# Performance work log

Measured on AMD Instinct MI355X. Metric: run time of the kernel, lower is better.

The kernel has to match this reference:

```python
import jax, jax.numpy as jnp
import numpy as np

B, SQ, SV = 2, 2048, 2048
DV, DQ, DK, DO, H = 1024, 1280, 1024, 1024, 16
DHK, DHO = DK // H, DO // H


def setup_inputs() -> dict:
    key = jax.random.key(0)
    ks = jax.random.split(key, 8)
    pre_value_key = jax.random.normal(ks[0], (B, SV, DV), jnp.float32)
    pre_query = jax.random.normal(ks[1], (B, SQ, DQ), jnp.float32)
    value_key_masks = (jax.random.uniform(ks[2], (B, SV)) < 0.9).astype(jnp.float32)
    value_key_counts = jnp.maximum(value_key_masks.sum(-1), 1.0)
    s = 0.02
    Wq = jax.random.normal(ks[3], (DQ, DK), jnp.float32) * s
    bq = jnp.zeros((DK,), jnp.float32)
    Wk = jax.random.normal(ks[4], (DV, DK), jnp.float32) * s
    bk = jnp.zeros((DK,), jnp.float32)
    Wv = jax.random.normal(ks[5], (DV, DO), jnp.float32) * s
    bv = jnp.zeros((DO,), jnp.float32)
    overall_gain = jnp.ones((1, H, 1, 1), jnp.float32)
    overall_bias = jnp.full((1, H, 1, 1), -10.0, jnp.float32)
    return dict(pre_value_key=pre_value_key, pre_query=pre_query,
                value_key_masks=value_key_masks, value_key_counts=value_key_counts,
                Wq=Wq, bq=bq, Wk=Wk, bk=bk, Wv=Wv, bv=bv,
                overall_gain=overall_gain, overall_bias=overall_bias)


def _heads(x, h):
    # (B, S, D) -> (B, h, S, D//h)
    b, s, d = x.shape
    return x.reshape(b, s, h, d // h).transpose(0, 2, 1, 3)


def reference(pre_value_key, pre_query, value_key_masks, value_key_counts,
              Wq, bq, Wk, bk, Wv, bv, overall_gain, overall_bias):
    q = _heads(pre_query @ Wq + bq, H)        # (B,H,SQ,DHK)
    k = _heads(pre_value_key @ Wk + bk, H)    # (B,H,SV,DHK)
    v = _heads(pre_value_key @ Wv + bv, H)    # (B,H,SV,DHO)

    scores = jnp.einsum('bhqd,bhkd->bhqk', q, k) / jnp.sqrt(jnp.float32(DHK))

    mask = value_key_masks  # (B,SV), 0/1 float
    # pooled-score sigmoid gate (cross-attn branch)
    pooled = (scores * mask[:, None, None, :]).sum(-1, keepdims=True)
    pooled = pooled / value_key_counts[:, None, None, None]
    overall_weight = jax.nn.sigmoid(pooled * overall_gain + overall_bias)  # (B,H,SQ,1)

    add_mask = jnp.where(mask == 0, -jnp.inf, 0.0).astype(scores.dtype)
    sm = jax.nn.softmax(scores + add_mask[:, None, None, :], axis=-1)
    h = jnp.einsum('bhqk,bhkd->bhqd', sm, v)  # (B,H,SQ,DHO)

    pq_split = _heads(pre_query[:, :, :DO], H)  # (B,H,SQ,DHO)
    out = pq_split * (1.0 - overall_weight) + h * overall_weight
    out = out.transpose(0, 2, 1, 3).reshape(B, SQ, DO)
    out = jnp.concatenate([out, pre_query[:, :, DO:]], axis=-1)  # (B,SQ,DQ)
    return out
```

## Files before the change

### kernel.cpp

```cpp
#include <hip/hip_runtime.h>

typedef __attribute__((ext_vector_type(8))) __bf16 bf16x8;
typedef __attribute__((ext_vector_type(4))) float f32x4;
typedef __attribute__((ext_vector_type(16))) float f32x16;
typedef __attribute__((ext_vector_type(4))) unsigned short us4;
typedef __attribute__((ext_vector_type(4))) unsigned int u32x4;
typedef __attribute__((ext_vector_type(2))) unsigned int u32x2;
typedef __attribute__((address_space(3))) void* as3vp;
typedef const __attribute__((address_space(1))) void* as1vp;

#define GLOAD_LDS16(g, l) __builtin_amdgcn_global_load_lds((as1vp)(g), (as3vp)(l), 16, 0, 0)

#if __has_builtin(__builtin_amdgcn_exp2f)
#define EXP2(x) __builtin_amdgcn_exp2f(x)
#else
#define EXP2(x) __expf((x) * 0.6931471805599453f)
#endif

__device__ __forceinline__ unsigned short f2bf(float f) {
  unsigned u = __builtin_bit_cast(unsigned, f);
  u += 0x7FFFu + ((u >> 16) & 1u);
  return (unsigned short)(u >> 16);
}
__device__ __forceinline__ float bf2f(unsigned short u) {
  return __builtin_bit_cast(float, (unsigned)u << 16);
}
__device__ __forceinline__ unsigned int pkbf(float a, float b) {
  unsigned int r;
  asm("v_cvt_pk_bf16_f32 %0, %1, %2" : "=v"(r) : "v"(a), "v"(b));
  return r;
}

__global__ void cvt_pq_tail(const float* __restrict__ x, unsigned short* __restrict__ y,
                            float* __restrict__ out) {
  const int i = blockIdx.x * 256 + threadIdx.x;
  if (i >= 1310720) return;
  float4 v = ((const float4*)x)[i];
  us4 o;
  o.x = f2bf(v.x); o.y = f2bf(v.y); o.z = f2bf(v.z); o.w = f2bf(v.w);
  ((us4*)y)[i] = o;
  if ((i % 320) >= 256) ((float4*)out)[i] = v;
}

__global__ void cvt_f32_bf16(const float* __restrict__ x, unsigned short* __restrict__ y, int n4) {
  int i = blockIdx.x * 256 + threadIdx.x;
  if (i >= n4) return;
  float4 v = ((const float4*)x)[i];
  us4 o;
  o.x = f2bf(v.x); o.y = f2bf(v.y); o.z = f2bf(v.z); o.w = f2bf(v.w);
  ((us4*)y)[i] = o;
}

__global__ void transpose_w3(const float* __restrict__ Wq, const float* __restrict__ Wk,
                             const float* __restrict__ Wv,
                             unsigned short* __restrict__ WqT, unsigned short* __restrict__ WkT,
                             unsigned short* __restrict__ WvT) {
  const int z = blockIdx.z;
  const int K = (z == 0) ? 1280 : 1024;
  if ((int)blockIdx.y * 32 >= K) return;
  const float* W = (z == 0) ? Wq : ((z == 1) ? Wk : Wv);
  unsigned short* WT = (z == 0) ? WqT : ((z == 1) ? WkT : WvT);
  __shared__ float t[32][33];
  const int tx = threadIdx.x & 31, ty = threadIdx.x >> 5;
  const int n0 = blockIdx.x * 32, k0 = blockIdx.y * 32;
#pragma unroll
  for (int i = 0; i < 32; i += 8)
    t[ty + i][tx] = W[(size_t)(k0 + ty + i) * 1024 + n0 + tx];
  __syncthreads();
#pragma unroll
  for (int i = 0; i < 32; i += 8)
    WT[(size_t)(n0 + ty + i) * K + k0 + tx] = f2bf(t[tx][ty + i]);
}

__global__ void km_reduce(const unsigned short* __restrict__ KF, const float* __restrict__ mask,
                          float* __restrict__ km, unsigned short* __restrict__ addm_bf) {
  if (blockIdx.x < 16) {
    const int i = blockIdx.x * 256 + threadIdx.x;
    addm_bf[i] = f2bf((mask[i] != 0.f) ? 0.f : -1e30f);
  }
  __shared__ float red[16][64];
  const int bh = blockIdx.x >> 3, chunk = blockIdx.x & 7;
  const int b = bh >> 4;
  const int dg = (threadIdx.x & 15) * 4, rg = threadIdx.x >> 4;
  const unsigned short* kfb = KF + ((size_t)bh << 17);
  const float* mr = mask + b * 2048;
  const int ks = dg >> 4, h5 = (dg >> 3) & 1, j0 = dg & 7;
  float a0 = 0.f, a1 = 0.f, a2 = 0.f, a3 = 0.f;
  const int kv0 = chunk * 256;
  for (int kv = kv0 + rg; kv < kv0 + 256; kv += 16) {
    const float mv = mr[kv];
    const int t = kv >> 6, rowin = kv & 63;
    const size_t off = (size_t)(((t * 4 + ks) * 2 + (rowin >> 5)) * 64 + h5 * 32 + (rowin & 31)) * 8 + j0;
    us4 kq = *(const us4*)(kfb + off);
    a0 = fmaf(mv, bf2f(kq.x), a0); a1 = fmaf(mv, bf2f(kq.y), a1);
    a2 = fmaf(mv, bf2f(kq.z), a2); a3 = fmaf(mv, bf2f(kq.w), a3);
  }
  red[rg][dg] = a0; red[rg][dg + 1] = a1; red[rg][dg + 2] = a2; red[rg][dg + 3] = a3;
  __syncthreads();
  if (threadIdx.x < 64) {
    float s = 0.f;
#pragma unroll
    for (int i = 0; i < 16; ++i) s += red[i][threadIdx.x];
    atomicAdd(&km[bh * 64 + threadIdx.x], s);
  }
}

__global__ __launch_bounds__(256, 2)
void gemm_all(const unsigned short* __restrict__ Aq,
              const unsigned short* __restrict__ Akv,
              const unsigned short* __restrict__ WqT,
              const unsigned short* __restrict__ WkT,
              const unsigned short* __restrict__ WvT,
              const float* __restrict__ bq,
              const float* __restrict__ bk,
              const float* __restrict__ bv,
              unsigned short* __restrict__ Qout,
              unsigned short* __restrict__ KFout,
              unsigned short* __restrict__ VFout) {
  __shared__ unsigned short sA[2][128 * 64];
  __shared__ unsigned short sB[2][128 * 64];
  const int z = blockIdx.z;
  const int KDIM = (z == 0) ? 1280 : 1024;
  const unsigned short* Arow = (z == 0) ? Aq : ((z == 1) ? WkT : Akv);
  const unsigned short* Brow = (z == 0) ? WqT : ((z == 1) ? Akv : WvT);
  const int rowA0 = (z == 1) ? blockIdx.y * 128 : blockIdx.x * 128;
  const int rowB0 = (z == 1) ? blockIdx.x * 128 : blockIdx.y * 128;

  const int tid = threadIdx.x, lane = tid & 63, w = tid >> 6;
  const int l15 = lane & 15, lhi = lane >> 4;
  const int wm = w >> 1, wn = w & 1;

  const f32x4 zv = {0.f, 0.f, 0.f, 0.f};
  f32x4 acc[4][4];
#pragma unroll
  for (int m = 0; m < 4; ++m)
#pragma unroll
    for (int n = 0; n < 4; ++n) acc[m][n] = zv;

  auto stage = [&](int buf, int kt) {
#pragma unroll
    for (int i = 0; i < 4; ++i) {
      const int c = i * 256 + tid;
      const int r = c >> 3, kc = ((c & 7) ^ (r & 7)) * 8;
      GLOAD_LDS16(Arow + (size_t)(rowA0 + r) * KDIM + kt + kc, &sA[buf][0] + c * 8);
      GLOAD_LDS16(Brow + (size_t)(rowB0 + r) * KDIM + kt + kc, &sB[buf][0] + c * 8);
    }
  };

  const int NT = KDIM / 64;
  stage(0, 0);
  __syncthreads();
  int cur = 0;
  for (int t = 0; t < NT; ++t) {
    if (t + 1 < NT) stage(cur ^ 1, (t + 1) * 64);
    const unsigned short* sAb = &sA[cur][0];
    const unsigned short* sBb = &sB[cur][0];
#pragma unroll
    for (int ks = 0; ks < 2; ++ks) {
      const int koS = (ks * 32 + lhi * 8) ^ ((l15 & 7) * 8);
      bf16x8 af[4], bfr[4];
#pragma unroll
      for (int m = 0; m < 4; ++m) af[m] = *(const bf16x8*)(sAb + (wm * 64 + m * 16 + l15) * 64 + koS);
#pragma unroll
      for (int n = 0; n < 4; ++n) bfr[n] = *(const bf16x8*)(sBb + (wn * 64 + n * 16 + l15) * 64 + koS);
#pragma unroll
      for (int m = 0; m < 4; ++m)
#pragma unroll
        for (int n = 0; n < 4; ++n)
          acc[m][n] = __builtin_amdgcn_mfma_f32_16x16x32_bf16(af[m], bfr[n], acc[m][n], 0, 0, 0);
    }
    __syncthreads();
    cur ^= 1;
  }

  if (z == 0) {
#pragma unroll
    for (int n = 0; n < 4; ++n) {
      const int gc = rowB0 + wn * 64 + n * 16 + l15;
      const float bb = bq[gc];
#pragma unroll
      for (int m = 0; m < 4; ++m) {
        const int gr0 = rowA0 + wm * 64 + m * 16 + lhi * 4;
#pragma unroll
        for (int r = 0; r < 4; ++r)
          Qout[(size_t)(gr0 + r) * 1024 + gc] = f2bf((acc[m][n][r] + bb) * 0.18033688f);
      }
    }
  } else if (z == 1) {
#pragma unroll
    for (int n = 0; n < 4; ++n) {
      const int gkv = rowB0 + wn * 64 + n * 16 + l15;
      const int b = gkv >> 11, kvl = gkv & 2047;
      const int t = kvl >> 6, rowin = kvl & 63;
      const int halfk = rowin >> 5, l31k = rowin & 31;
#pragma unroll
      for (int m = 0; m < 4; ++m) {
        const int gch = rowA0 + wm * 64 + m * 16 + lhi * 4;
        const f32x4 bb = *(const f32x4*)(bk + gch);
        const int h = gch >> 6, chh = gch & 63;
        const int ks = chh >> 4, h5k = (chh >> 3) & 1, j0 = chh & 7;
        const size_t off = ((size_t)(b * 16 + h) << 17) +
                           (size_t)(((t * 4 + ks) * 2 + halfk) * 64 + h5k * 32 + l31k) * 8 + j0;
        u32x2 st;
        st.x = pkbf(acc[m][n][0] + bb[0], acc[m][n][1] + bb[1]);
        st.y = pkbf(acc[m][n][2] + bb[2], acc[m][n][3] + bb[3]);
        *(u32x2*)(KFout + off) = st;
      }
    }
  } else {
    __syncthreads();
    unsigned* tb = (unsigned*)&sA[0][0];
#pragma unroll
    for (int n = 0; n < 4; ++n) {
      const int gcL = wn * 64 + n * 16 + l15;
      const float bb = bv[rowB0 + gcL];
#pragma unroll
      for (int m = 0; m < 4; ++m) {
#pragma unroll
        for (int k = 0; k < 2; ++k) {
          const int grPair = wm * 32 + m * 8 + lhi * 2 + k;
          const int W = (grPair & 3) | ((((grPair >> 2) ^ gcL) & 15) << 2);
          tb[gcL * 64 + W] = pkbf(acc[m][n][2 * k] + bb, acc[m][n][2 * k + 1] + bb);
        }
      }
    }
    __syncthreads();
    const int b_ = rowA0 >> 11;
#pragma unroll
    for (int it = 0; it < 8; ++it) {
      const int c = it * 256 + tid;
      const int gcL = (c & 63) + ((c >> 10) << 6);
      const int u = (c >> 6) & 15;
      const int W4 = (u ^ gcL) & 15;
      u32x4 o = *(const u32x4*)(tb + gcL * 64 + W4 * 4);
      const int kv0 = (rowA0 & 2047) + u * 8;
      const int ch = rowB0 + gcL;
      const int hh2 = ch >> 6, d = ch & 63;
      const int t2 = kv0 >> 6, ks2 = (kv0 >> 4) & 3, h5v = (kv0 >> 3) & 1;
      const size_t off = ((size_t)(b_ * 16 + hh2) << 17) +
                         (size_t)(((t2 * 4 + ks2) * 2 + (d >> 5)) * 64 + h5v * 32 + (d & 31)) * 8;
      *(u32x4*)(VFout + off) = o;
    }
  }
}

__global__ __launch_bounds__(256, 2)
void attn_fused(const unsigned short* __restrict__ Q,
                const unsigned short* __restrict__ KF,
                const unsigned short* __restrict__ VF,
                const unsigned short* __restrict__ addm_bf,
                const float* __restrict__ km,
                const float* __restrict__ counts,
                const float* __restrict__ gain,
                const float* __restrict__ gbias,
                const float* __restrict__ pq,
                float* __restrict__ out) {
  __shared__ float sOT[4 * 2048];

  const int tid = threadIdx.x, lane = tid & 63, w = tid >> 6;
  const int l31 = lane & 31, h5 = lane >> 5;
  const int f = blockIdx.x;
  const int qt = (f >> 3) & 15;
  const int bh = (f & 7) + 8 * (f >> 7);
  const int b = bh >> 4, hh = bh & 15;
  const int q0 = qt * 128;

  bf16x8 qf[4];
  {
    const unsigned short* qp = Q + (size_t)(b * 2048 + q0 + w * 32 + l31) * 1024 + hh * 64 + h5 * 8;
#pragma unroll
    for (int ks = 0; ks < 4; ++ks) qf[ks] = *(const bf16x8*)(qp + ks * 16);
  }

  float pl_s = 0.f;
  {
    const float* kmp = km + (b * 16 + hh) * 64 + h5 * 8;
#pragma unroll
    for (int ks = 0; ks < 4; ++ks) {
      f32x4 ka = *(const f32x4*)(kmp + ks * 16);
      f32x4 kb4 = *(const f32x4*)(kmp + ks * 16 + 4);
#pragma unroll
      for (int j = 0; j < 4; ++j)
        pl_s += (float)qf[ks][j] * ka[j] + (float)qf[ks][j + 4] * kb4[j];
    }
    float ta = pl_s, tb = pl_s;
    asm("v_permlane32_swap_b32 %0, %1" : "+v"(ta), "+v"(tb));
    pl_s = ta + tb;
  }

  const unsigned short* KFb = KF + ((size_t)bh << 17) + lane * 8;
  const unsigned short* VFb = VF + ((size_t)bh << 17) + lane * 8;
  const unsigned short* amb = addm_bf + b * 2048;

  bf16x8 qone;
  {
    u32x4 fq = {h5 ? 0u : 0x3F80u, 0u, 0u, 0u};
    qone = __builtin_bit_cast(bf16x8, fq);
  }

  f32x16 o0, o1, l_vec;
#pragma unroll
  for (int r = 0; r < 16; ++r) { o0[r] = 0.f; o1[r] = 0.f; l_vec[r] = 0.f; }
  float m_ = -1e30f;

  bf16x8 kA[8], kB[8], vf[8];
  auto ldK = [&](int t, bf16x8 (&kf)[8]) {
    const unsigned short* p = KFb + (size_t)t * 4096;
#pragma unroll
    for (int i = 0; i < 8; ++i) kf[i] = *(const bf16x8*)(p + i * 512);
  };
  auto ldV = [&](int t, bf16x8 (&vv)[8]) {
    const unsigned short* p = VFb + (size_t)t * 4096;
#pragma unroll
    for (int i = 0; i < 8; ++i) vv[i] = *(const bf16x8*)(p + i * 512);
  };

  auto body = [&](int t, bf16x8 (&kf)[8], bf16x8 (&nkf)[8], bool ln) {
    ldV(t, vf);
    if (ln) ldK(t + 1, nkf);
    const unsigned short am0 = amb[t * 64 + l31];
    const unsigned short am1 = amb[t * 64 + 32 + l31];

    f32x16 s0, s1;
#pragma unroll
    for (int r = 0; r < 16; ++r) { s0[r] = 0.f; s1[r] = 0.f; }

#pragma unroll
    for (int ks = 0; ks < 4; ++ks) {
      s0 = __builtin_amdgcn_mfma_f32_32x32x16_bf16(kf[ks * 2], qf[ks], s0, 0, 0, 0);
      s1 = __builtin_amdgcn_mfma_f32_32x32x16_bf16(kf[ks * 2 + 1], qf[ks], s1, 0, 0, 0);
    }
    {
      u32x4 fa0 = {h5 ? 0u : (unsigned)am0, 0u, 0u, 0u};
      u32x4 fa1 = {h5 ? 0u : (unsigned)am1, 0u, 0u, 0u};
      s0 = __builtin_amdgcn_mfma_f32_32x32x16_bf16(__builtin_bit_cast(bf16x8, fa0), qone, s0, 0, 0, 0);
      s1 = __builtin_amdgcn_mfma_f32_32x32x16_bf16(__builtin_bit_cast(bf16x8, fa1), qone, s1, 0, 0, 0);
    }

    f32x16 mx;
#pragma unroll
    for (int r = 0; r < 16; ++r) mx[r] = fmaxf(s0[r], s1[r]);
    float t8[8];
#pragma unroll
    for (int r = 0; r < 8; ++r) t8[r] = fmaxf(mx[r], mx[r + 8]);
    float tp = fmaxf(fmaxf(fmaxf(t8[0], t8[1]), fmaxf(t8[2], t8[3])),
                     fmaxf(fmaxf(t8[4], t8[5]), fmaxf(t8[6], t8[7])));
    {
      float ta = tp, tb = tp;
      asm("v_permlane32_swap_b32 %0, %1" : "+v"(ta), "+v"(tb));
      tp = fmaxf(ta, tb);
    }
    if (__any(tp > m_ + 11.0f)) {
      const float mnew = fmaxf(m_, tp);
      const float corr = EXP2(m_ - mnew);
      m_ = mnew;
      l_vec *= corr; o0 *= corr; o1 *= corr;
    }

    f32x16 p0, p1;
#pragma unroll
    for (int r = 0; r < 16; ++r) p0[r] = EXP2(s0[r] - m_);
#pragma unroll
    for (int r = 0; r < 16; ++r) p1[r] = EXP2(s1[r] - m_);
    l_vec += p0; l_vec += p1;

    bf16x8 pfs[4];
    {
      unsigned x0 = pkbf(p0[0], p0[1]), y0 = pkbf(p0[2], p0[3]);
      unsigned z0 = pkbf(p0[4], p0[5]), w0 = pkbf(p0[6], p0[7]);
      asm("v_permlane32_swap_b32 %0, %1" : "+v"(x0), "+v"(z0));
      asm("v_permlane32_swap_b32 %0, %1" : "+v"(y0), "+v"(w0));
      u32x4 f0 = {x0, y0, z0, w0};
      pfs[0] = __builtin_bit_cast(bf16x8, f0);
      unsigned x1 = pkbf(p0[8], p0[9]), y1 = pkbf(p0[10], p0[11]);
      unsigned z1 = pkbf(p0[12], p0[13]), w1 = pkbf(p0[14], p0[15]);
      asm("v_permlane32_swap_b32 %0, %1" : "+v"(x1), "+v"(z1));
      asm("v_permlane32_swap_b32 %0, %1" : "+v"(y1), "+v"(w1));
      u32x4 f1 = {x1, y1, z1, w1};
      pfs[1] = __builtin_bit_cast(bf16x8, f1);
      unsigned x2 = pkbf(p1[0], p1[1]), y2 = pkbf(p1[2], p1[3]);
      unsigned z2 = pkbf(p1[4], p1[5]), w2 = pkbf(p1[6], p1[7]);
      asm("v_permlane32_swap_b32 %0, %1" : "+v"(x2), "+v"(z2));
      asm("v_permlane32_swap_b32 %0, %1" : "+v"(y2), "+v"(w2));
      u32x4 f2 = {x2, y2, z2, w2};
      pfs[2] = __builtin_bit_cast(bf16x8, f2);
      unsigned x3 = pkbf(p1[8], p1[9]), y3 = pkbf(p1[10], p1[11]);
      unsigned z3 = pkbf(p1[12], p1[13]), w3 = pkbf(p1[14], p1[15]);
      asm("v_permlane32_swap_b32 %0, %1" : "+v"(x3), "+v"(z3));
      asm("v_permlane32_swap_b32 %0, %1" : "+v"(y3), "+v"(w3));
      u32x4 f3 = {x3, y3, z3, w3};
      pfs[3] = __builtin_bit_cast(bf16x8, f3);
    }

#pragma unroll
    for (int ks = 0; ks < 4; ++ks) {
      o0 = __builtin_amdgcn_mfma_f32_32x32x16_bf16(vf[ks * 2], pfs[ks], o0, 0, 0, 0);
      o1 = __builtin_amdgcn_mfma_f32_32x32x16_bf16(vf[ks * 2 + 1], pfs[ks], o1, 0, 0, 0);
    }
  };

  ldK(0, kA);
#pragma unroll 1
  for (int t = 0; t < 32; t += 2) {
    body(t, kA, kB, true);
    body(t + 1, kB, kA, t + 2 < 32);
  }

  float l_s;
  {
    float a[8];
#pragma unroll
    for (int r = 0; r < 8; ++r) a[r] = l_vec[r] + l_vec[r + 8];
    l_s = ((a[0] + a[1]) + (a[2] + a[3])) + ((a[4] + a[5]) + (a[6] + a[7]));
    float ta = l_s, tb = l_s;
    asm("v_permlane32_swap_b32 %0, %1" : "+v"(ta), "+v"(tb));
    l_s = ta + tb;
  }
  const float po = pl_s * 0.6931471805599453f / counts[b];
  const float wgv = 1.f / (1.f + __expf(-(po * gain[hh] + gbias[hh])));
  const float invl = 1.f / l_s;

  float* myOT = sOT + w * 2048;
#pragma unroll
  for (int r = 0; r < 16; ++r) {
    const int d0 = (r & 3) + 8 * (r >> 2) + 4 * h5;
    myOT[d0 * 32 + (l31 ^ (d0 & 31))] = o0[r] * invl;
    const int d1 = d0 + 32;
    myOT[d1 * 32 + (l31 ^ (d1 & 31))] = o1[r] * invl;
  }
  __syncthreads();
  const size_t rowbase = (size_t)(b * 2048 + q0 + w * 32) * 1280 + hh * 64 + lane;
  const float* pqrow = pq + rowbase;
  float* outrow = out + rowbase;
#pragma unroll 4
  for (int i = 0; i < 32; ++i) {
    const float hval = myOT[lane * 32 + (i ^ (lane & 31))];
    const float wgrow = __shfl(wgv, i, 64);
    const float pv = pqrow[(size_t)i * 1280];
    outrow[(size_t)i * 1280] = fmaf(hval - pv, wgrow, pv);
  }
}

extern "C" void kernel_launch(void* const* d_in, const int* in_sizes, int n_in,
                              void* d_out, int out_size, void* d_ws, size_t ws_size,
                              hipStream_t stream) {
  const float* pre_vk = (const float*)d_in[0];
  const float* pre_q  = (const float*)d_in[1];
  const float* vmask  = (const float*)d_in[2];
  const float* vcnt   = (const float*)d_in[3];
  const float* Wq = (const float*)d_in[4];
  const float* bq = (const float*)d_in[5];
  const float* Wk = (const float*)d_in[6];
  const float* bk = (const float*)d_in[7];
  const float* Wv = (const float*)d_in[8];
  const float* bv = (const float*)d_in[9];
  const float* gain  = (const float*)d_in[10];
  const float* gbias = (const float*)d_in[11];
  float* out = (float*)d_out;

  char* ws = (char*)d_ws;
  unsigned short* pq_bf = (unsigned short*)(ws);
  unsigned short* pv_bf = (unsigned short*)(ws + 10485760);
  unsigned short* WqT   = (unsigned short*)(ws + 18874368);
  unsigned short* WkT   = (unsigned short*)(ws + 21495808);
  unsigned short* WvT   = (unsigned short*)(ws + 23592960);
  unsigned short* Qb    = (unsigned short*)(ws + 25690112);
  unsigned short* KFb   = (unsigned short*)(ws + 34078720);
  unsigned short* VFb   = (unsigned short*)(ws + 42467328);
  float*          kmb   = (float*)(ws + 50855936);
  unsigned short* addmb = (unsigned short*)(ws + 50864128);

  hipMemsetAsync(kmb, 0, 2 * 16 * 64 * sizeof(float), stream);
  cvt_pq_tail<<<5120, 256, 0, stream>>>(pre_q, pq_bf, out);
  cvt_f32_bf16<<<4096, 256, 0, stream>>>(pre_vk, pv_bf, 1048576);
  transpose_w3<<<dim3(32, 40, 3), 256, 0, stream>>>(Wq, Wk, Wv, WqT, WkT, WvT);
  gemm_all<<<dim3(32, 8, 3), 256, 0, stream>>>(pq_bf, pv_bf, WqT, WkT, WvT, bq, bk, bv, Qb, KFb, VFb);
  km_reduce<<<256, 256, 0, stream>>>(KFb, vmask, kmb, addmb);
  attn_fused<<<512, 256, 0, stream>>>(Qb, KFb, VFb, addmb, kmb, vcnt, gain, gbias, pre_q, out);
}
```

Measured before the change: 128.1 us.

## Split KV loop across two wave groups per block and merge softmax partials

Doubles the block to 512 threads. Each query group of 32 rows is processed by two waves, each taking alternating KV tiles, and their partial max, sum and output are merged through LDS with a log-sum-exp rescale. This halves the serial KV loop per wave and raises occupancy to hide memory latency. In exchange it adds LDS traffic and extra syncs, and the tighter launch bounds risk register spills.

```diff
diff --git a/kernel.cpp b/kernel.cpp
--- a/kernel.cpp
+++ b/kernel.cpp
@@ -244,7 +244,7 @@
   }
 }
 
-__global__ __launch_bounds__(256, 2)
+__global__ __launch_bounds__(512, 4)
 void attn_fused(const unsigned short* __restrict__ Q,
                 const unsigned short* __restrict__ KF,
                 const unsigned short* __restrict__ VF,
@@ -256,9 +256,11 @@
                 const float* __restrict__ pq,
                 float* __restrict__ out) {
   __shared__ float sOT[4 * 2048];
+  __shared__ float ex[1024];
 
   const int tid = threadIdx.x, lane = tid & 63, w = tid >> 6;
   const int l31 = lane & 31, h5 = lane >> 5;
+  const int qg = w & 3, half = w >> 2;
   const int f = blockIdx.x;
   const int qt = (f >> 3) & 15;
   const int bh = (f & 7) + 8 * (f >> 7);
@@ -267,7 +269,7 @@
 
   bf16x8 qf[4];
   {
-    const unsigned short* qp = Q + (size_t)(b * 2048 + q0 + w * 32 + l31) * 1024 + hh * 64 + h5 * 8;
+    const unsigned short* qp = Q + (size_t)(b * 2048 + q0 + qg * 32 + l31) * 1024 + hh * 64 + h5 * 8;
 #pragma unroll
     for (int ks = 0; ks < 4; ++ks) qf[ks] = *(const bf16x8*)(qp + ks * 16);
   }
@@ -317,7 +319,7 @@
 
   auto body = [&](int t, bf16x8 (&kf)[8], bf16x8 (&nkf)[8], bool ln) {
     ldV(t, vf);
-    if (ln) ldK(t + 1, nkf);
+    if (ln) ldK(t + 2, nkf);
     const unsigned short am0 = amb[t * 64 + l31];
     const unsigned short am1 = amb[t * 64 + 32 + l31];
 
@@ -399,42 +401,67 @@
     }
   };
 
-  ldK(0, kA);
+  ldK(half, kA);
 #pragma unroll 1
-  for (int t = 0; t < 32; t += 2) {
-    body(t, kA, kB, true);
-    body(t + 1, kB, kA, t + 2 < 32);
-  }
-
-  float l_s;
+  for (int j = 0; j < 16; j += 2) {
+    body(2 * j + half, kA, kB, true);
+    body(2 * (j + 1) + half, kB, kA, j + 2 < 16);
+  }
+
+  float l_part;
   {
     float a[8];
 #pragma unroll
     for (int r = 0; r < 8; ++r) a[r] = l_vec[r] + l_vec[r + 8];
-    l_s = ((a[0] + a[1]) + (a[2] + a[3])) + ((a[4] + a[5]) + (a[6] + a[7]));
-    float ta = l_s, tb = l_s;
+    l_part = ((a[0] + a[1]) + (a[2] + a[3])) + ((a[4] + a[5]) + (a[6] + a[7]));
+    float ta = l_part, tb = l_part;
     asm("v_permlane32_swap_b32 %0, %1" : "+v"(ta), "+v"(tb));
-    l_s = ta + tb;
-  }
+    l_part = ta + tb;
+  }
+
+  ex[(w * 64 + lane) * 2] = m_;
+  ex[(w * 64 + lane) * 2 + 1] = l_part;
+  __syncthreads();
+  const int pw = w ^ 4;
+  const float pm = ex[(pw * 64 + lane) * 2];
+  const float plp = ex[(pw * 64 + lane) * 2 + 1];
+  const float mM = fmaxf(m_, pm);
+  const float lM = l_part * EXP2(m_ - mM) + plp * EXP2(pm - mM);
+  const float sc = EXP2(m_ - mM) / lM;
+
   const float po = pl_s * 0.6931471805599453f / counts[b];
   const float wgv = 1.f / (1.f + __expf(-(po * gain[hh] + gbias[hh])));
-  const float invl = 1.f / l_s;
-
-  float* myOT = sOT + w * 2048;
-#pragma unroll
-  for (int r = 0; r < 16; ++r) {
-    const int d0 = (r & 3) + 8 * (r >> 2) + 4 * h5;
-    myOT[d0 * 32 + (l31 ^ (d0 & 31))] = o0[r] * invl;
-    const int d1 = d0 + 32;
-    myOT[d1 * 32 + (l31 ^ (d1 & 31))] = o1[r] * invl;
+
+  float* sOTq = sOT + qg * 2048;
+  if (half == 1) {
+#pragma unroll
+    for (int r = 0; r < 16; ++r) {
+      const int d0 = (r & 3) + 8 * (r >> 2) + 4 * h5;
+      sOTq[d0 * 32 + (l31 ^ (d0 & 31))] = o0[r] * sc;
+      const int d1 = d0 + 32;
+      sOTq[d1 * 32 + (l31 ^ (d1 & 31))] = o1[r] * sc;
+    }
   }
   __syncthreads();
-  const size_t rowbase = (size_t)(b * 2048 + q0 + w * 32) * 1280 + hh * 64 + lane;
+  if (half == 0) {
+#pragma unroll
+    for (int r = 0; r < 16; ++r) {
+      const int d0 = (r & 3) + 8 * (r >> 2) + 4 * h5;
+      const int i0 = d0 * 32 + (l31 ^ (d0 & 31));
+      sOTq[i0] += o0[r] * sc;
+      const int d1 = d0 + 32;
+      const int i1 = d1 * 32 + (l31 ^ (d1 & 31));
+      sOTq[i1] += o1[r] * sc;
+    }
+  }
+  __syncthreads();
+
+  const size_t rowbase = (size_t)(b * 2048 + q0 + qg * 32) * 1280 + hh * 64 + lane;
   const float* pqrow = pq + rowbase;
   float* outrow = out + rowbase;
 #pragma unroll 4
-  for (int i = 0; i < 32; ++i) {
-    const float hval = myOT[lane * 32 + (i ^ (lane & 31))];
+  for (int i = half * 16; i < half * 16 + 16; ++i) {
+    const float hval = sOTq[lane * 32 + (i ^ (lane & 31))];
     const float wgrow = __shfl(wgv, i, 64);
     const float pv = pqrow[(size_t)i * 1280];
     outrow[(size_t)i * 1280] = fmaf(hval - pv, wgrow, pv);
@@ -476,5 +503,5 @@
   transpose_w3<<<dim3(32, 40, 3), 256, 0, stream>>>(Wq, Wk, Wv, WqT, WkT, WvT);
   gemm_all<<<dim3(32, 8, 3), 256, 0, stream>>>(pq_bf, pv_bf, WqT, WkT, WvT, bq, bk, bv, Qb, KFb, VFb);
   km_reduce<<<256, 256, 0, stream>>>(KFb, vmask, kmb, addmb);
-  attn_fused<<<512, 256, 0, stream>>>(Qb, KFb, VFb, addmb, kmb, vcnt, gain, gbias, pre_q, out);
-}
+  attn_fused<<<512, 512, 0, stream>>>(Qb, KFb, VFb, addmb, kmb, vcnt, gain, gbias, pre_q, out);
+}
```

Result: slower. 353.7 us (+176.2%).
